# Kernel tuning notes

Measured on AMD Instinct MI355X. Metric: run time of the kernel, lower is better.

The kernel has to match this reference:

```python
import jax, jax.numpy as jnp
import numpy as np

H = 8          # num_heads
L = 256        # lifting_dim
DH = L // H    # head dim


def setup_inputs() -> dict:
    key = jax.random.key(0)
    ks = jax.random.split(key, 32)
    B, N, E = 4, 16384, 65536
    Dn, De, Dg = 128, 64, 32

    def lin_w(k, din, dout):
        return jax.random.normal(k, (din, dout), jnp.float32) * (din ** -0.5)

    inp = {
        "node_features": jax.random.normal(ks[0], (B, N, Dn), jnp.float32),
        "edge_features": jax.random.normal(ks[1], (B, E, De), jnp.float32),
        "energy": jax.random.normal(ks[2], (Dg,), jnp.float32),
        "W_node": lin_w(ks[3], Dn, L), "b_node": jnp.zeros((L,), jnp.float32),
        "W_edge": lin_w(ks[4], De, L), "b_edge": jnp.zeros((L,), jnp.float32),
        "W_graph": lin_w(ks[5], Dg, L), "b_graph": jnp.zeros((L,), jnp.float32),
        "Wq": lin_w(ks[6], L, L), "bq": jnp.zeros((L,), jnp.float32),
        # stacked per-hetero-type key/value projections: [3, L, L]
        "Wk": jnp.stack([lin_w(ks[7 + i], L, L) for i in range(3)]),
        "bk": jnp.zeros((3, L), jnp.float32),
        "Wv": jnp.stack([lin_w(ks[10 + i], L, L) for i in range(3)]),
        "bv": jnp.zeros((3, L), jnp.float32),
        "W_out": lin_w(ks[13], L, L), "b_out": jnp.zeros((L,), jnp.float32),
    }
    return inp


def _heads(x, B, T):
    # [B,T,L] -> [B,H,T,DH]
    return x.reshape(B, T, H, DH).transpose(0, 2, 1, 3)


def reference(node_features, edge_features, energy,
              W_node, b_node, W_edge, b_edge, W_graph, b_graph,
              Wq, bq, Wk, bk, Wv, bv, W_out, b_out):
    B, N, _ = node_features.shape
    lifted_nodes = node_features @ W_node + b_node            # [B,N,L]
    lifted_edges = edge_features @ W_edge + b_edge            # [B,E,L]
    lifted_graph = jnp.broadcast_to(energy, (B, 1, energy.shape[0])) @ W_graph + b_graph  # [B,1,L]

    hetero = [lifted_nodes, lifted_edges, lifted_graph]

    q = _heads(lifted_nodes @ Wq + bq, B, N)                  # [B,H,N,DH]
    q = jax.nn.softmax(q, axis=-1)

    out = None
    # NOTE: faithful to the original, `out` is overwritten each iteration,
    # so only the last hetero feature (graph) determines the output.
    for i in range(3):
        h = hetero[i]
        T = h.shape[1]
        k = jax.nn.softmax(_heads(h @ Wk[i] + bk[i], B, T), axis=-1)  # [B,H,T,DH]
        v = _heads(h @ Wv[i] + bv[i], B, T)                           # [B,H,T,DH]
        k_sum = k.sum(axis=-2, keepdims=True)                          # [B,H,1,DH]
        d_inv = 1.0 / jnp.clip((q * k_sum).sum(axis=-1, keepdims=True), 1e-8)  # [B,H,N,1]
        kv = jnp.einsum("bhtd,bhte->bhde", k, v)                       # [B,H,DH,DH]
        out = q + jnp.einsum("bhnd,bhde->bhne", q, kv) * d_inv         # [B,H,N,DH]

    out = out.transpose(0, 2, 1, 3).reshape(B, N, L)
    return out @ W_out + b_out
```

## Files before the change

kernel.cpp:

```cpp
#include <hip/hip_runtime.h>
#include <hip/hip_bf16.h>
#include <cstdint>
#include <cstddef>


typedef __attribute__((ext_vector_type(8))) short short8;
typedef __attribute__((ext_vector_type(4))) float floatx4;

using bf16 = __hip_bfloat16;

static constexpr int Mrows = 65536;
static constexpr int Lcols = 256;

static __device__ __forceinline__ short f2bs(float x) {
  bf16 h = __float2bfloat16(x);
  return *reinterpret_cast<short*>(&h);
}

__global__ void k_setup(const float* __restrict__ W_node,
                        const float* __restrict__ Wq,
                        const float* __restrict__ W_out,
                        const float* __restrict__ energy,
                        const float* __restrict__ W_graph,
                        const float* __restrict__ b_graph,
                        const float* __restrict__ Wk,
                        const float* __restrict__ bk,
                        const float* __restrict__ Wv,
                        const float* __restrict__ bv,
                        const float* __restrict__ b_node,
                        const float* __restrict__ bq,
                        short* __restrict__ wnq_t,
                        short* __restrict__ wto_t,
                        float* __restrict__ klbuf,
                        float* __restrict__ vvec,
                        float* __restrict__ bnq) {
  const int b = blockIdx.x;
  const int t = threadIdx.x;

  if (b < 256) {
    __shared__ float wqc[256];
    const int j = b;
    wqc[t] = Wq[t * 256 + j];
    __syncthreads();
    if (t < 128) {
      const float* wr = W_node + t * 256;
      float acc = 0.f;
#pragma unroll 8
      for (int l = 0; l < 256; ++l) acc += wr[l] * wqc[l];
      wnq_t[j * 128 + t] = f2bs(acc);
    }
  } else if (b < 512) {
    const int r = b - 256;
    wto_t[t * 256 + r] = f2bs(W_out[r * 256 + t]);
  } else {
    __shared__ float ev[32];
    __shared__ float r0[256], r1[256], r2[256];
    const int j = b - 512, d = t;
    if (d < 32) ev[d] = energy[d];
    __syncthreads();

    float lgd = b_graph[d];
#pragma unroll
    for (int e = 0; e < 32; ++e) lgd += ev[e] * W_graph[e * 256 + d];

    r0[d] = lgd * Wk[2 * 65536 + d * 256 + j];
    r1[d] = lgd * Wv[2 * 65536 + d * 256 + j];
    r2[d] = b_node[d] * Wq[d * 256 + j];
    __syncthreads();
    for (int s = 128; s > 0; s >>= 1) {
      if (d < s) { r0[d] += r0[d + s]; r1[d] += r1[d + s]; r2[d] += r2[d + s]; }
      __syncthreads();
    }
    if (d == 0) {
      klbuf[j] = r0[0] + bk[512 + j];
      vvec[j]  = r1[0] + bv[512 + j];
      bnq[j]   = r2[0] + bq[j];
    }
  }
}

__global__ __launch_bounds__(256, 4)
void k_fused(const float* __restrict__ nf,
             const short* __restrict__ wnq,
             const short* __restrict__ wto,
             const float* __restrict__ klbuf,
             const float* __restrict__ bnq,
             const float* __restrict__ vvec,
             const float* __restrict__ b_out,
             float* __restrict__ out) {
  constexpr int AS_STR = 136;
  constexpr int PS_STR = 264;
  __shared__ short smem[64 * PS_STR];
  __shared__ float kl[256];
  __shared__ float kv[256];

  const int t = threadIdx.x;
  const int lane = t & 63;
  const int l15 = lane & 15;
  const int lhi = lane >> 4;
  const int cw = (t >> 6) * 64;
  const int rowBase = blockIdx.x * 64;

  kl[t] = klbuf[t];

  {
    const int row = t >> 2;
    const int c0 = (t & 3) << 5;
    const float* src = nf + (size_t)(rowBase + row) * 128 + c0;
    short tmp[32];
#pragma unroll
    for (int i = 0; i < 8; ++i) {
      float4 f = *(const float4*)(src + i * 4);
      tmp[i * 4 + 0] = f2bs(f.x); tmp[i * 4 + 1] = f2bs(f.y);
      tmp[i * 4 + 2] = f2bs(f.z); tmp[i * 4 + 3] = f2bs(f.w);
    }
#pragma unroll
    for (int i = 0; i < 4; ++i)
      *(short8*)(&smem[row * AS_STR + c0 + i * 8]) = *(short8*)(&tmp[i * 8]);
  }
  __syncthreads();

  {
    const int h0 = t & ~31;
    float mx = -1e30f;
#pragma unroll 8
    for (int i = 0; i < 32; ++i) mx = fmaxf(mx, kl[h0 + i]);
    float s = 0.f;
#pragma unroll 8
    for (int i = 0; i < 32; ++i) s += __expf(kl[h0 + i] - mx);
    kv[t] = __expf(kl[t] - mx) / s;
  }

  floatx4 acc[4][4];
#pragma unroll
  for (int m = 0; m < 4; ++m)
#pragma unroll
    for (int n = 0; n < 4; ++n) acc[m][n] = (floatx4){0.f, 0.f, 0.f, 0.f};

  {
    const short* wb = wnq + (cw + l15) * 128 + lhi * 8;
#pragma unroll
    for (int kc = 0; kc < 4; ++kc) {
      short8 af[4], bfv[4];
#pragma unroll
      for (int n = 0; n < 4; ++n)
        bfv[n] = *(const short8*)(wb + n * 16 * 128 + kc * 32);
#pragma unroll
      for (int m = 0; m < 4; ++m)
        af[m] = *(const short8*)(&smem[(m * 16 + l15) * AS_STR + kc * 32 + lhi * 8]);
#pragma unroll
      for (int m = 0; m < 4; ++m)
#pragma unroll
        for (int n = 0; n < 4; ++n)
          acc[m][n] = __builtin_amdgcn_mfma_f32_16x16x32_bf16(af[m], bfv[n],
                                                              acc[m][n], 0, 0, 0);
    }
  }
  __syncthreads();

#pragma unroll
  for (int tt = 0; tt < 2; ++tt) {
    const int col0 = cw + tt * 32 + l15;
    const int col1 = col0 + 16;
    const float b0 = bnq[col0], b1 = bnq[col1];
    const float k0v = kv[col0], k1v = kv[col1];
    const float v0v = vvec[col0], v1v = vvec[col1];
#pragma unroll
    for (int m = 0; m < 4; ++m) {
      const int row0 = m * 16 + lhi * 4;
#pragma unroll
      for (int r = 0; r < 4; ++r) {
        float e0 = __expf(acc[m][2 * tt][r] + b0);
        float e1 = __expf(acc[m][2 * tt + 1][r] + b1);
        float s = e0 + e1;
        float du = e0 * k0v + e1 * k1v;
#pragma unroll
        for (int msk = 1; msk <= 8; msk <<= 1) {
          s += __shfl_xor(s, msk);
          du += __shfl_xor(du, msk);
        }
        float inv = 1.0f / s;
        float d = du * inv;
        float ratio = d / fmaxf(d, 1e-8f);
        smem[(row0 + r) * PS_STR + col0] = f2bs(e0 * inv + v0v * ratio);
        smem[(row0 + r) * PS_STR + col1] = f2bs(e1 * inv + v1v * ratio);
      }
    }
  }
#pragma unroll
  for (int m = 0; m < 4; ++m)
#pragma unroll
    for (int n = 0; n < 4; ++n) acc[m][n] = (floatx4){0.f, 0.f, 0.f, 0.f};
  __syncthreads();

  {
    const short* wb = wto + (cw + l15) * 256 + lhi * 8;
#pragma unroll
    for (int kc = 0; kc < 8; ++kc) {
      short8 af[4], bfv[4];
#pragma unroll
      for (int n = 0; n < 4; ++n)
        bfv[n] = *(const short8*)(wb + n * 16 * 256 + kc * 32);
#pragma unroll
      for (int m = 0; m < 4; ++m)
        af[m] = *(const short8*)(&smem[(m * 16 + l15) * PS_STR + kc * 32 + lhi * 8]);
#pragma unroll
      for (int m = 0; m < 4; ++m)
#pragma unroll
        for (int n = 0; n < 4; ++n)
          acc[m][n] = __builtin_amdgcn_mfma_f32_16x16x32_bf16(af[m], bfv[n],
                                                              acc[m][n], 0, 0, 0);
    }
  }

#pragma unroll
  for (int n = 0; n < 4; ++n) {
    const int col = cw + n * 16 + l15;
    const float bb = b_out[col];
#pragma unroll
    for (int m = 0; m < 4; ++m) {
      const int row0 = rowBase + m * 16 + lhi * 4;
#pragma unroll
      for (int r = 0; r < 4; ++r)
        out[(size_t)(row0 + r) * Lcols + col] = acc[m][n][r] + bb;
    }
  }
}

extern "C" void kernel_launch(void* const* d_in, const int* in_sizes, int n_in,
                              void* d_out, int out_size, void* d_ws, size_t ws_size,
                              hipStream_t stream) {
  const float* node_features = (const float*)d_in[0];
  const float* energy  = (const float*)d_in[2];
  const float* W_node  = (const float*)d_in[3];
  const float* b_node  = (const float*)d_in[4];
  const float* W_graph = (const float*)d_in[7];
  const float* b_graph = (const float*)d_in[8];
  const float* Wq      = (const float*)d_in[9];
  const float* bq      = (const float*)d_in[10];
  const float* Wk      = (const float*)d_in[11];
  const float* bk      = (const float*)d_in[12];
  const float* Wv      = (const float*)d_in[13];
  const float* bv      = (const float*)d_in[14];
  const float* W_out   = (const float*)d_in[15];
  const float* b_out   = (const float*)d_in[16];

  char* ws = (char*)d_ws;
  short* wnq_t = (short*)(ws);
  short* wto_t = (short*)(ws + 65536);
  float* klbuf = (float*)(ws + 196608);
  float* vvec  = (float*)(ws + 197632);
  float* bnq   = (float*)(ws + 198656);

  k_setup<<<dim3(768), dim3(256), 0, stream>>>(
      W_node, Wq, W_out, energy, W_graph, b_graph, Wk, bk, Wv, bv,
      b_node, bq, wnq_t, wto_t, klbuf, vvec, bnq);

  k_fused<<<dim3(Mrows / 64), dim3(256), 0, stream>>>(
      node_features, wnq_t, wto_t, klbuf, bnq, vvec, b_out, (float*)d_out);
}
```

Measured before the change: 196.8 us.

## Halve fused-kernel row tile, raise occupancy, and move key softmax into setup

The fused kernel now handles 32 rows per block instead of 64, with half the shared memory and accumulators, and its launch bound asks for 8 waves per SIMD instead of 4. The goal is more resident blocks to hide global-load latency. The per-block key softmax moves into the setup kernel, which now handles one head per block with a two-stage reduction, cutting its blocks from 768 to 520. In exchange, each weight fragment fetched feeds half as many MFMAs, so weight traffic per row doubles, and register pressure under the tighter bound could cause spills.

```diff
diff --git a/kernel.cpp b/kernel.cpp
--- a/kernel.cpp
+++ b/kernel.cpp
@@ -31,7 +31,7 @@
                         const float* __restrict__ bq,
                         short* __restrict__ wnq_t,
                         short* __restrict__ wto_t,
-                        float* __restrict__ klbuf,
+                        float* __restrict__ kvec,
                         float* __restrict__ vvec,
                         float* __restrict__ bnq) {
   const int b = blockIdx.x;
@@ -54,86 +54,97 @@
     wto_t[t * 256 + r] = f2bs(W_out[r * 256 + t]);
   } else {
     __shared__ float ev[32];
+    __shared__ float lg[256];
     __shared__ float r0[256], r1[256], r2[256];
-    const int j = b - 512, d = t;
-    if (d < 32) ev[d] = energy[d];
-    __syncthreads();
-
-    float lgd = b_graph[d];
-#pragma unroll
-    for (int e = 0; e < 32; ++e) lgd += ev[e] * W_graph[e * 256 + d];
-
-    r0[d] = lgd * Wk[2 * 65536 + d * 256 + j];
-    r1[d] = lgd * Wv[2 * 65536 + d * 256 + j];
-    r2[d] = b_node[d] * Wq[d * 256 + j];
-    __syncthreads();
-    for (int s = 128; s > 0; s >>= 1) {
-      if (d < s) { r0[d] += r0[d + s]; r1[d] += r1[d + s]; r2[d] += r2[d + s]; }
-      __syncthreads();
-    }
-    if (d == 0) {
-      klbuf[j] = r0[0] + bk[512 + j];
-      vvec[j]  = r1[0] + bv[512 + j];
-      bnq[j]   = r2[0] + bq[j];
-    }
-  }
-}
-
-__global__ __launch_bounds__(256, 4)
+    __shared__ float klh[32];
+    const int h = b - 512;
+    if (t < 32) ev[t] = energy[t];
+    __syncthreads();
+
+    {
+      float lgd = b_graph[t];
+#pragma unroll
+      for (int e = 0; e < 32; ++e) lgd += ev[e] * W_graph[e * 256 + t];
+      lg[t] = lgd;
+    }
+    __syncthreads();
+
+    const int g = t >> 5;
+    const int c = t & 31;
+    const int j = h * 32 + c;
+    float p0 = 0.f, p1 = 0.f, p2 = 0.f;
+#pragma unroll
+    for (int i = 0; i < 32; ++i) {
+      const int d = g * 32 + i;
+      const float l = lg[d];
+      p0 += l * Wk[2 * 65536 + d * 256 + j];
+      p1 += l * Wv[2 * 65536 + d * 256 + j];
+      p2 += b_node[d] * Wq[d * 256 + j];
+    }
+    r0[t] = p0; r1[t] = p1; r2[t] = p2;
+    __syncthreads();
+    if (t < 32) {
+      float s0 = 0.f, s1 = 0.f, s2 = 0.f;
+#pragma unroll
+      for (int gg = 0; gg < 8; ++gg) {
+        s0 += r0[gg * 32 + c]; s1 += r1[gg * 32 + c]; s2 += r2[gg * 32 + c];
+      }
+      klh[c] = s0 + bk[512 + j];
+      vvec[j] = s1 + bv[512 + j];
+      bnq[j]  = s2 + bq[j];
+    }
+    __syncthreads();
+    if (t < 32) {
+      float mx = -1e30f;
+#pragma unroll
+      for (int i = 0; i < 32; ++i) mx = fmaxf(mx, klh[i]);
+      float s = 0.f;
+#pragma unroll
+      for (int i = 0; i < 32; ++i) s += __expf(klh[i] - mx);
+      kvec[j] = __expf(klh[c] - mx) / s;
+    }
+  }
+}
+
+__global__ __launch_bounds__(256, 8)
 void k_fused(const float* __restrict__ nf,
              const short* __restrict__ wnq,
              const short* __restrict__ wto,
-             const float* __restrict__ klbuf,
              const float* __restrict__ bnq,
+             const float* __restrict__ kvec,
              const float* __restrict__ vvec,
              const float* __restrict__ b_out,
              float* __restrict__ out) {
   constexpr int AS_STR = 136;
   constexpr int PS_STR = 264;
-  __shared__ short smem[64 * PS_STR];
-  __shared__ float kl[256];
-  __shared__ float kv[256];
+  __shared__ short smem[32 * PS_STR];
 
   const int t = threadIdx.x;
   const int lane = t & 63;
   const int l15 = lane & 15;
   const int lhi = lane >> 4;
   const int cw = (t >> 6) * 64;
-  const int rowBase = blockIdx.x * 64;
-
-  kl[t] = klbuf[t];
+  const int rowBase = blockIdx.x * 32;
 
   {
-    const int row = t >> 2;
-    const int c0 = (t & 3) << 5;
+    const int row = t >> 3;
+    const int c0 = (t & 7) << 4;
     const float* src = nf + (size_t)(rowBase + row) * 128 + c0;
-    short tmp[32];
-#pragma unroll
-    for (int i = 0; i < 8; ++i) {
+    short tmp[16];
+#pragma unroll
+    for (int i = 0; i < 4; ++i) {
       float4 f = *(const float4*)(src + i * 4);
       tmp[i * 4 + 0] = f2bs(f.x); tmp[i * 4 + 1] = f2bs(f.y);
       tmp[i * 4 + 2] = f2bs(f.z); tmp[i * 4 + 3] = f2bs(f.w);
     }
-#pragma unroll
-    for (int i = 0; i < 4; ++i)
-      *(short8*)(&smem[row * AS_STR + c0 + i * 8]) = *(short8*)(&tmp[i * 8]);
+    *(short8*)(&smem[row * AS_STR + c0]) = *(short8*)(&tmp[0]);
+    *(short8*)(&smem[row * AS_STR + c0 + 8]) = *(short8*)(&tmp[8]);
   }
   __syncthreads();
 
-  {
-    const int h0 = t & ~31;
-    float mx = -1e30f;
-#pragma unroll 8
-    for (int i = 0; i < 32; ++i) mx = fmaxf(mx, kl[h0 + i]);
-    float s = 0.f;
-#pragma unroll 8
-    for (int i = 0; i < 32; ++i) s += __expf(kl[h0 + i] - mx);
-    kv[t] = __expf(kl[t] - mx) / s;
-  }
-
-  floatx4 acc[4][4];
-#pragma unroll
-  for (int m = 0; m < 4; ++m)
+  floatx4 acc[2][4];
+#pragma unroll
+  for (int m = 0; m < 2; ++m)
 #pragma unroll
     for (int n = 0; n < 4; ++n) acc[m][n] = (floatx4){0.f, 0.f, 0.f, 0.f};
 
@@ -141,15 +152,15 @@
     const short* wb = wnq + (cw + l15) * 128 + lhi * 8;
 #pragma unroll
     for (int kc = 0; kc < 4; ++kc) {
-      short8 af[4], bfv[4];
+      short8 af[2], bfv[4];
 #pragma unroll
       for (int n = 0; n < 4; ++n)
         bfv[n] = *(const short8*)(wb + n * 16 * 128 + kc * 32);
 #pragma unroll
-      for (int m = 0; m < 4; ++m)
+      for (int m = 0; m < 2; ++m)
         af[m] = *(const short8*)(&smem[(m * 16 + l15) * AS_STR + kc * 32 + lhi * 8]);
 #pragma unroll
-      for (int m = 0; m < 4; ++m)
+      for (int m = 0; m < 2; ++m)
 #pragma unroll
         for (int n = 0; n < 4; ++n)
           acc[m][n] = __builtin_amdgcn_mfma_f32_16x16x32_bf16(af[m], bfv[n],
@@ -163,10 +174,10 @@
     const int col0 = cw + tt * 32 + l15;
     const int col1 = col0 + 16;
     const float b0 = bnq[col0], b1 = bnq[col1];
-    const float k0v = kv[col0], k1v = kv[col1];
+    const float k0v = kvec[col0], k1v = kvec[col1];
     const float v0v = vvec[col0], v1v = vvec[col1];
 #pragma unroll
-    for (int m = 0; m < 4; ++m) {
+    for (int m = 0; m < 2; ++m) {
       const int row0 = m * 16 + lhi * 4;
 #pragma unroll
       for (int r = 0; r < 4; ++r) {
@@ -188,7 +199,7 @@
     }
   }
 #pragma unroll
-  for (int m = 0; m < 4; ++m)
+  for (int m = 0; m < 2; ++m)
 #pragma unroll
     for (int n = 0; n < 4; ++n) acc[m][n] = (floatx4){0.f, 0.f, 0.f, 0.f};
   __syncthreads();
@@ -197,15 +208,15 @@
     const short* wb = wto + (cw + l15) * 256 + lhi * 8;
 #pragma unroll
     for (int kc = 0; kc < 8; ++kc) {
-      short8 af[4], bfv[4];
+      short8 af[2], bfv[4];
 #pragma unroll
       for (int n = 0; n < 4; ++n)
         bfv[n] = *(const short8*)(wb + n * 16 * 256 + kc * 32);
 #pragma unroll
-      for (int m = 0; m < 4; ++m)
+      for (int m = 0; m < 2; ++m)
         af[m] = *(const short8*)(&smem[(m * 16 + l15) * PS_STR + kc * 32 + lhi * 8]);
 #pragma unroll
-      for (int m = 0; m < 4; ++m)
+      for (int m = 0; m < 2; ++m)
 #pragma unroll
         for (int n = 0; n < 4; ++n)
           acc[m][n] = __builtin_amdgcn_mfma_f32_16x16x32_bf16(af[m], bfv[n],
@@ -218,7 +229,7 @@
     const int col = cw + n * 16 + l15;
     const float bb = b_out[col];
 #pragma unroll
-    for (int m = 0; m < 4; ++m) {
+    for (int m = 0; m < 2; ++m) {
       const int row0 = rowBase + m * 16 + lhi * 4;
 #pragma unroll
       for (int r = 0; r < 4; ++r)
@@ -248,14 +259,14 @@
   char* ws = (char*)d_ws;
   short* wnq_t = (short*)(ws);
   short* wto_t = (short*)(ws + 65536);
-  float* klbuf = (float*)(ws + 196608);
+  float* kvec  = (float*)(ws + 196608);
   float* vvec  = (float*)(ws + 197632);
   float* bnq   = (float*)(ws + 198656);
 
-  k_setup<<<dim3(768), dim3(256), 0, stream>>>(
+  k_setup<<<dim3(520), dim3(256), 0, stream>>>(
       W_node, Wq, W_out, energy, W_graph, b_graph, Wk, bk, Wv, bv,
-      b_node, bq, wnq_t, wto_t, klbuf, vvec, bnq);
-
-  k_fused<<<dim3(Mrows / 64), dim3(256), 0, stream>>>(
-      node_features, wnq_t, wto_t, klbuf, bnq, vvec, b_out, (float*)d_out);
-}
+      b_node, bq, wnq_t, wto_t, kvec, vvec, bnq);
+
+  k_fused<<<dim3(Mrows / 32), dim3(256), 0, stream>>>(
+      node_features, wnq_t, wto_t, bnq, kvec, vvec, b_out, (float*)d_out);
+}
```

After: 214.4 us. 8.9% more time.

## Drop the graph-key normalizer, stage output through LDS, simplify setup reductions

Applied to the files above, without the earlier changes.

There is only one graph token, so k_sum equals k and the normalizer d/max(d,1e-8) evaluates to 1 whenever d is at least 1e-8. The fused kernel therefore drops the key softmax, the dot-product shuffles and the division, and adds vvec directly. The final stores are staged through shared memory so each row goes out as full float4 writes instead of scattered 4-byte stores. The setup kernel now uses 8 blocks with per-thread partial sums in place of 256 tree reductions. The risk is that the clip is no longer applied if d ever falls below 1e-8, and the staging adds extra barriers.

```diff
diff --git a/kernel.cpp b/kernel.cpp
--- a/kernel.cpp
+++ b/kernel.cpp
@@ -31,7 +31,6 @@
                         const float* __restrict__ bq,
                         short* __restrict__ wnq_t,
                         short* __restrict__ wto_t,
-                        float* __restrict__ klbuf,
                         float* __restrict__ vvec,
                         float* __restrict__ bnq) {
   const int b = blockIdx.x;
@@ -54,27 +53,40 @@
     wto_t[t * 256 + r] = f2bs(W_out[r * 256 + t]);
   } else {
     __shared__ float ev[32];
-    __shared__ float r0[256], r1[256], r2[256];
-    const int j = b - 512, d = t;
-    if (d < 32) ev[d] = energy[d];
-    __syncthreads();
-
-    float lgd = b_graph[d];
-#pragma unroll
-    for (int e = 0; e < 32; ++e) lgd += ev[e] * W_graph[e * 256 + d];
-
-    r0[d] = lgd * Wk[2 * 65536 + d * 256 + j];
-    r1[d] = lgd * Wv[2 * 65536 + d * 256 + j];
-    r2[d] = b_node[d] * Wq[d * 256 + j];
-    __syncthreads();
-    for (int s = 128; s > 0; s >>= 1) {
-      if (d < s) { r0[d] += r0[d + s]; r1[d] += r1[d + s]; r2[d] += r2[d + s]; }
-      __syncthreads();
-    }
-    if (d == 0) {
-      klbuf[j] = r0[0] + bk[512 + j];
-      vvec[j]  = r1[0] + bv[512 + j];
-      bnq[j]   = r2[0] + bq[j];
+    __shared__ float lg[256];
+    __shared__ float r1[256], r2[256];
+    const int h = b - 512;
+    if (t < 32) ev[t] = energy[t];
+    __syncthreads();
+
+    {
+      float lgd = b_graph[t];
+#pragma unroll
+      for (int e = 0; e < 32; ++e) lgd += ev[e] * W_graph[e * 256 + t];
+      lg[t] = lgd;
+    }
+    __syncthreads();
+
+    const int g = t >> 5;
+    const int c = t & 31;
+    const int j = h * 32 + c;
+    float p1 = 0.f, p2 = 0.f;
+#pragma unroll
+    for (int i = 0; i < 32; ++i) {
+      const int d = g * 32 + i;
+      p1 += lg[d] * Wv[2 * 65536 + d * 256 + j];
+      p2 += b_node[d] * Wq[d * 256 + j];
+    }
+    r1[t] = p1; r2[t] = p2;
+    __syncthreads();
+    if (t < 32) {
+      float s1 = 0.f, s2 = 0.f;
+#pragma unroll
+      for (int gg = 0; gg < 8; ++gg) {
+        s1 += r1[gg * 32 + c]; s2 += r2[gg * 32 + c];
+      }
+      vvec[j] = s1 + bv[512 + j];
+      bnq[j]  = s2 + bq[j];
     }
   }
 }
@@ -83,16 +95,15 @@
 void k_fused(const float* __restrict__ nf,
              const short* __restrict__ wnq,
              const short* __restrict__ wto,
-             const float* __restrict__ klbuf,
              const float* __restrict__ bnq,
              const float* __restrict__ vvec,
              const float* __restrict__ b_out,
              float* __restrict__ out) {
   constexpr int AS_STR = 136;
   constexpr int PS_STR = 264;
+  constexpr int FO_STR = 260;
   __shared__ short smem[64 * PS_STR];
-  __shared__ float kl[256];
-  __shared__ float kv[256];
+  float* fsm = (float*)smem;
 
   const int t = threadIdx.x;
   const int lane = t & 63;
@@ -101,8 +112,6 @@
   const int cw = (t >> 6) * 64;
   const int rowBase = blockIdx.x * 64;
 
-  kl[t] = klbuf[t];
-
   {
     const int row = t >> 2;
     const int c0 = (t & 3) << 5;
@@ -120,17 +129,6 @@
   }
   __syncthreads();
 
-  {
-    const int h0 = t & ~31;
-    float mx = -1e30f;
-#pragma unroll 8
-    for (int i = 0; i < 32; ++i) mx = fmaxf(mx, kl[h0 + i]);
-    float s = 0.f;
-#pragma unroll 8
-    for (int i = 0; i < 32; ++i) s += __expf(kl[h0 + i] - mx);
-    kv[t] = __expf(kl[t] - mx) / s;
-  }
-
   floatx4 acc[4][4];
 #pragma unroll
   for (int m = 0; m < 4; ++m)
@@ -163,7 +161,6 @@
     const int col0 = cw + tt * 32 + l15;
     const int col1 = col0 + 16;
     const float b0 = bnq[col0], b1 = bnq[col1];
-    const float k0v = kv[col0], k1v = kv[col1];
     const float v0v = vvec[col0], v1v = vvec[col1];
 #pragma unroll
     for (int m = 0; m < 4; ++m) {
@@ -173,17 +170,11 @@
         float e0 = __expf(acc[m][2 * tt][r] + b0);
         float e1 = __expf(acc[m][2 * tt + 1][r] + b1);
         float s = e0 + e1;
-        float du = e0 * k0v + e1 * k1v;
-#pragma unroll
-        for (int msk = 1; msk <= 8; msk <<= 1) {
-          s += __shfl_xor(s, msk);
-          du += __shfl_xor(du, msk);
-        }
+#pragma unroll
+        for (int msk = 1; msk <= 8; msk <<= 1) s += __shfl_xor(s, msk);
         float inv = 1.0f / s;
-        float d = du * inv;
-        float ratio = d / fmaxf(d, 1e-8f);
-        smem[(row0 + r) * PS_STR + col0] = f2bs(e0 * inv + v0v * ratio);
-        smem[(row0 + r) * PS_STR + col1] = f2bs(e1 * inv + v1v * ratio);
+        smem[(row0 + r) * PS_STR + col0] = f2bs(e0 * inv + v0v);
+        smem[(row0 + r) * PS_STR + col1] = f2bs(e1 * inv + v1v);
       }
     }
   }
@@ -213,16 +204,33 @@
     }
   }
 
-#pragma unroll
-  for (int n = 0; n < 4; ++n) {
-    const int col = cw + n * 16 + l15;
-    const float bb = b_out[col];
-#pragma unroll
-    for (int m = 0; m < 4; ++m) {
-      const int row0 = rowBase + m * 16 + lhi * 4;
-#pragma unroll
-      for (int r = 0; r < 4; ++r)
-        out[(size_t)(row0 + r) * Lcols + col] = acc[m][n][r] + bb;
+  float bb[4];
+#pragma unroll
+  for (int n = 0; n < 4; ++n) bb[n] = b_out[cw + n * 16 + l15];
+
+#pragma unroll
+  for (int c = 0; c < 2; ++c) {
+    __syncthreads();
+#pragma unroll
+    for (int mm = 0; mm < 2; ++mm) {
+      const int m = c * 2 + mm;
+#pragma unroll
+      for (int n = 0; n < 4; ++n) {
+        const int col = cw + n * 16 + l15;
+        const int row0 = mm * 16 + lhi * 4;
+#pragma unroll
+        for (int r = 0; r < 4; ++r)
+          fsm[(row0 + r) * FO_STR + col] = acc[m][n][r] + bb[n];
+      }
+    }
+    __syncthreads();
+#pragma unroll
+    for (int i = 0; i < 8; ++i) {
+      const int f = i * 256 + t;
+      const int row = f >> 6;
+      const int c4 = (f & 63) << 2;
+      float4 vv = *(const float4*)(&fsm[row * FO_STR + c4]);
+      *(float4*)(&out[(size_t)(rowBase + c * 32 + row) * Lcols + c4]) = vv;
     }
   }
 }
@@ -248,14 +256,13 @@
   char* ws = (char*)d_ws;
   short* wnq_t = (short*)(ws);
   short* wto_t = (short*)(ws + 65536);
-  float* klbuf = (float*)(ws + 196608);
-  float* vvec  = (float*)(ws + 197632);
-  float* bnq   = (float*)(ws + 198656);
-
-  k_setup<<<dim3(768), dim3(256), 0, stream>>>(
+  float* vvec  = (float*)(ws + 196608);
+  float* bnq   = (float*)(ws + 197632);
+
+  k_setup<<<dim3(520), dim3(256), 0, stream>>>(
       W_node, Wq, W_out, energy, W_graph, b_graph, Wk, bk, Wv, bv,
-      b_node, bq, wnq_t, wto_t, klbuf, vvec, bnq);
+      b_node, bq, wnq_t, wto_t, vvec, bnq);
 
   k_fused<<<dim3(Mrows / 64), dim3(256), 0, stream>>>(
-      node_features, wnq_t, wto_t, klbuf, bnq, vvec, b_out, (float*)d_out);
-}
+      node_features, wnq_t, wto_t, bnq, vvec, b_out, (float*)d_out);
+}
```

Result: faster. 190.1 us (-3.4%).
